# Performance work log

Measured on AMD Instinct MI355X. Metric: run time of the kernel, lower is better.

## Reference

```python
import jax, jax.numpy as jnp
import numpy as np

DIM = 1024
HEADS = 16
SCALE = DIM ** -0.5  # note: source scales by full dim, not head dim


def setup_inputs() -> dict:
    key = jax.random.key(0)
    k1, k2, k3 = jax.random.split(key, 3)
    b, n = 2, 2048
    x = jax.random.normal(k1, (b, n, DIM), dtype=jnp.float32)
    w_qkv = jax.random.normal(k2, (3 * DIM, DIM), dtype=jnp.float32) * (DIM ** -0.5)
    w_out = jax.random.normal(k3, (DIM, DIM), dtype=jnp.float32) * (DIM ** -0.5)
    b_out = jnp.zeros((DIM,), dtype=jnp.float32)
    return {"x": x, "w_qkv": w_qkv, "w_out": w_out, "b_out": b_out}


def reference(x, w_qkv, w_out, b_out):
    b, n, d = x.shape
    h = HEADS
    hd = d // h
    # torch Linear: y = x @ W.T
    qkv = x @ w_qkv.T  # [b, n, 3d]
    q, k, v = jnp.split(qkv, 3, axis=-1)
    # reshape to [b, h, n, hd]
    def to_heads(t):
        return t.reshape(b, n, h, hd).transpose(0, 2, 1, 3)
    q, k, v = to_heads(q), to_heads(k), to_heads(v)
    dots = jnp.einsum('bhqd,bhkd->bhqk', q, k) * SCALE
    attn = jax.nn.softmax(dots, axis=-1)
    out = jnp.einsum('bhqk,bhkd->bhqd', attn, v)
    out = out.transpose(0, 2, 1, 3).reshape(b, n, d)
    return out @ w_out.T + b_out
```

## Files before the change

kernel.cpp:

```cpp
#include <hip/hip_runtime.h>

typedef __attribute__((ext_vector_type(8))) _Float16 half8;
typedef __attribute__((ext_vector_type(4))) _Float16 half4;
typedef __attribute__((ext_vector_type(2))) __fp16 fp16x2;
typedef __attribute__((ext_vector_type(4))) float f32x4;
typedef __attribute__((ext_vector_type(4))) unsigned int u32x4;
typedef __attribute__((ext_vector_type(2))) unsigned int u32x2;

#define NSEQ 2048
#define DIMM 1024
#define NH   16
#define HD   64

typedef const void __attribute__((address_space(1))) gvoid_t;
typedef void __attribute__((address_space(3))) svoid_t;

__device__ __forceinline__ void gload_lds16(const void* g, void* l) {
  __builtin_amdgcn_global_load_lds((gvoid_t*)g, (svoid_t*)l, 16, 0, 0);
}

union H2U { fp16x2 h; unsigned int u; };

__global__ __launch_bounds__(256) void cvt_all(const float* __restrict__ x,
                                               const float* __restrict__ wqkv,
                                               const float* __restrict__ wout,
                                               _Float16* __restrict__ xh,
                                               _Float16* __restrict__ wqkvh,
                                               _Float16* __restrict__ wouth) {
  int i = blockIdx.x * 256 + threadIdx.x;
  const float* src;
  _Float16* dst;
  int off;
  if (i < 524288) { src = x; dst = xh; off = i; }
  else if (i < 917504) { src = wqkv; dst = wqkvh; off = i - 524288; }
  else { src = wout; dst = wouth; off = i - 917504; }
  const float4* p = (const float4*)src + (size_t)off * 2;
  float4 v0 = p[0], v1 = p[1];
  half8 h;
  h[0] = (_Float16)v0.x; h[1] = (_Float16)v0.y; h[2] = (_Float16)v0.z; h[3] = (_Float16)v0.w;
  h[4] = (_Float16)v1.x; h[5] = (_Float16)v1.y; h[6] = (_Float16)v1.z; h[7] = (_Float16)v1.w;
  *((half8*)dst + off) = h;
}

#define QSCALE 0.0450843450f

union SmemQ {
  struct { _Float16 A[3 * 8192]; _Float16 B[3 * 8192]; } m;
  _Float16 t[128 * 264];
};

__global__ __launch_bounds__(512, 1) void gemm_qkv(const _Float16* __restrict__ x,
                                                   const _Float16* __restrict__ wqkv,
                                                   _Float16* __restrict__ qh,
                                                   _Float16* __restrict__ kh,
                                                   _Float16* __restrict__ vt) {
  __shared__ SmemQ sh;
  const int bid = blockIdx.x;
  const int swz = (bid & 7) * 24 + (bid >> 3);
  const int bm = swz & 15, bn = swz >> 4;
  const int am0 = bm * 256, bn0 = bn * 256;
  const int tid = threadIdx.x, w = tid >> 6, lane = tid & 63;
  const int g = lane >> 4, ln = lane & 15;
  const int wmq = (w >> 2) * 128, wnq = (w & 3) * 64;

  const int srl = tid >> 2;
  const int ssl = (tid & 3) ^ ((srl >> 1) & 3);
  const int dsto = tid * 8;

#define QSTG(buf, kt, ht)                                                           \
  {                                                                                 \
    if ((ht) < 2) {                                                                 \
      gload_lds16(x + (size_t)(am0 + (ht) * 128 + srl) * 1024 + (kt) * 32 + ssl * 8,\
                  sh.m.A + (buf) * 8192 + (ht) * 4096 + dsto);                      \
    } else {                                                                        \
      gload_lds16(wqkv + (size_t)(bn0 + ((ht) - 2) * 128 + srl) * 1024 +            \
                      (kt) * 32 + ssl * 8,                                          \
                  sh.m.B + (buf) * 8192 + ((ht) - 2) * 4096 + dsto);                \
    }                                                                               \
  }

  f32x4 acc[8][4];
#pragma unroll
  for (int i = 0; i < 8; ++i)
#pragma unroll
    for (int j = 0; j < 4; ++j) acc[i][j] = (f32x4){0.f, 0.f, 0.f, 0.f};

#pragma unroll
  for (int ht = 0; ht < 4; ++ht) QSTG(0, 0, ht)
#pragma unroll
  for (int ht = 0; ht < 4; ++ht) QSTG(1, 1, ht)

  for (int t = 0; t < 32; ++t) {
    const int buf = t % 3;
    const int sbuf = (t + 2) % 3;
    if (t < 31) {
      asm volatile("s_waitcnt vmcnt(4)" ::: "memory");
    } else {
      asm volatile("s_waitcnt vmcnt(0)" ::: "memory");
    }
    __builtin_amdgcn_s_barrier();
    const _Float16* Ab = sh.m.A + buf * 8192;
    const _Float16* Bb = sh.m.B + buf * 8192;
    half8 bf[4];
#pragma unroll
    for (int ni = 0; ni < 4; ++ni) {
      const int r = wnq + ni * 16 + ln;
      bf[ni] = *(const half8*)(Bb + r * 32 + ((g ^ ((r >> 1) & 3)) << 3));
    }
#pragma unroll
    for (int p = 0; p < 4; ++p) {
      const int r0 = wmq + (2 * p) * 16 + ln;
      const int r1 = wmq + (2 * p + 1) * 16 + ln;
      half8 af0 = *(const half8*)(Ab + r0 * 32 + ((g ^ ((r0 >> 1) & 3)) << 3));
      half8 af1 = *(const half8*)(Ab + r1 * 32 + ((g ^ ((r1 >> 1) & 3)) << 3));
      __builtin_amdgcn_s_setprio(1);
#pragma unroll
      for (int ni = 0; ni < 4; ++ni) {
        acc[2 * p][ni]     = __builtin_amdgcn_mfma_f32_16x16x32_f16(af0, bf[ni], acc[2 * p][ni], 0, 0, 0);
        acc[2 * p + 1][ni] = __builtin_amdgcn_mfma_f32_16x16x32_f16(af1, bf[ni], acc[2 * p + 1][ni], 0, 0, 0);
      }
      __builtin_amdgcn_s_setprio(0);
      if (t < 30) QSTG(sbuf, t + 2, p)
      if (p < 3) __builtin_amdgcn_s_barrier();
    }
  }

  const int sec = bn >> 2;
  const int cbase = (bn & 3) * 256;

  if (sec < 2) {
    _Float16* dst = (sec == 0) ? qh : kh;
    const float scale = (sec == 0) ? QSCALE : 1.0f;
#pragma unroll
    for (int mi = 0; mi < 8; ++mi) {
      const int row = am0 + wmq + mi * 16 + g * 4;
      const int bidx = row >> 11, nidx = row & 2047;
#pragma unroll
      for (int ni = 0; ni < 4; ++ni) {
        const int col = cbase + wnq + ni * 16 + ln;
        const int h = col >> 6, d = col & 63;
        _Float16* p = dst + ((size_t)(bidx * NH + h) * NSEQ + nidx) * HD + d;
#pragma unroll
        for (int r = 0; r < 4; ++r) p[r * HD] = (_Float16)(acc[mi][ni][r] * scale);
      }
    }
  } else {
    const int bidx = bm >> 3;
    const int n0 = (bm * 256) & 2047;
#pragma unroll
    for (int hc = 0; hc < 2; ++hc) {
      __syncthreads();
      if (((w & 3) >> 1) == hc) {
#pragma unroll
        for (int mi = 0; mi < 8; ++mi)
#pragma unroll
          for (int ni = 0; ni < 4; ++ni) {
            const int cl = wnq + ni * 16 + ln - hc * 128;
            const int rowl = wmq + mi * 16 + g * 4;
#pragma unroll
            for (int r = 0; r < 4; ++r)
              sh.t[cl * 264 + rowl + r] = (_Float16)acc[mi][ni][r];
          }
      }
      __syncthreads();
#pragma unroll
      for (int i = 0; i < 8; ++i) {
        const int ci = i * 512 + tid;
        const int cl = ci >> 5, npos = (ci & 31) * 8;
        const int col = cbase + hc * 128 + cl;
        const int h = col >> 6, d = col & 63;
        u32x4 v = *(const u32x4*)(sh.t + cl * 264 + npos);
        *(u32x4*)(vt + ((size_t)(bidx * NH + h) * HD + d) * NSEQ + n0 + npos) = v;
      }
    }
  }
}

__global__ __launch_bounds__(256, 2) void attn_fwd(const _Float16* __restrict__ qg,
                                                   const _Float16* __restrict__ kg,
                                                   const _Float16* __restrict__ vg,
                                                   _Float16* __restrict__ ao) {
  __shared__ _Float16 Ks[3][64 * 64];
  __shared__ _Float16 Vs[3][64 * 64];
  __shared__ float Lred[2][128];

  const int bid = blockIdx.x;
  const int swz = (bid & 7) * 64 + (bid >> 3);
  const int bh = swz >> 4, qt = swz & 15;
  const int tid = threadIdx.x, w = tid >> 6, lane = tid & 63;
  const int g = lane >> 4, ln = lane & 15;
  const int sw8 = ln & 7;
  const int qh2 = w >> 1, kh2 = w & 1;

  const _Float16* qp = qg + (size_t)bh * NSEQ * HD;
  const _Float16* kp = kg + (size_t)bh * NSEQ * HD;
  const _Float16* vp = vg + (size_t)bh * HD * NSEQ;

  const int qr0 = qt * 128;

  half8 qf[4][2];
#pragma unroll
  for (int qb = 0; qb < 4; ++qb)
#pragma unroll
    for (int dk = 0; dk < 2; ++dk)
      qf[qb][dk] = *(const half8*)(qp + (size_t)(qr0 + qh2 * 64 + qb * 16 + ln) * HD + dk * 32 + g * 8);
  asm volatile("" ::: "memory");

  const int rsub = lane >> 3;
  const int csw = ((lane & 7) ^ rsub) << 3;
  const int c0 = 2 * w;
  const int R0 = c0 * 8 + rsub, R1 = R0 + 8;
  const int ks0 = 32 * (R0 >> 5) + 8 * ((R0 >> 2) & 3) + 4 * ((R0 >> 4) & 1) + (R0 & 3);
  const int ks1 = 32 * (R1 >> 5) + 8 * ((R1 >> 2) & 3) + 4 * ((R1 >> 4) & 1) + (R1 & 3);

#define ASTAGE(buf, tt)                                                             \
  {                                                                                 \
    const _Float16* kt_ = kp + (size_t)(tt) * 64 * HD;                              \
    gload_lds16(kt_ + (size_t)ks0 * HD + csw, &Ks[buf][c0 * 512]);                  \
    gload_lds16(kt_ + (size_t)ks1 * HD + csw, &Ks[buf][(c0 + 1) * 512]);            \
    gload_lds16(vp + (size_t)(c0 * 8 + rsub) * NSEQ + (tt) * 64 + csw,              \
                &Vs[buf][c0 * 512]);                                                \
    gload_lds16(vp + (size_t)((c0 + 1) * 8 + rsub) * NSEQ + (tt) * 64 + csw,        \
                &Vs[buf][(c0 + 1) * 512]);                                          \
  }

  ASTAGE(0, 0);
  ASTAGE(1, 1);

  float lsum[4] = {0.f, 0.f, 0.f, 0.f};
  f32x4 oacc[4][4];
#pragma unroll
  for (int sd = 0; sd < 4; ++sd)
#pragma unroll
    for (int qb = 0; qb < 4; ++qb) oacc[sd][qb] = (f32x4){0.f, 0.f, 0.f, 0.f};
  const f32x4 fz = (f32x4){0.f, 0.f, 0.f, 0.f};

#define TILE_BODY(kbuf, vbuf)                                                       \
  {                                                                                 \
    const _Float16* kb_ = (kbuf);                                                   \
    const _Float16* vb_ = (vbuf);                                                   \
    f32x4 sacc[2][4];                                                               \
    __builtin_amdgcn_s_setprio(1);                                                  \
    _Pragma("unroll")                                                               \
    for (int s = 0; s < 2; ++s) {                                                   \
      const _Float16* kr = kb_ + (kh2 * 32 + s * 16 + ln) * 64;                     \
      half8 kf0 = *(const half8*)(kr + ((g ^ sw8) << 3));                           \
      half8 kf1 = *(const half8*)(kr + (((4 + g) ^ sw8) << 3));                     \
      _Pragma("unroll")                                                             \
      for (int qb = 0; qb < 4; ++qb) {                                              \
        sacc[s][qb] = __builtin_amdgcn_mfma_f32_16x16x32_f16(kf0, qf[qb][0], fz, 0, 0, 0);          \
        sacc[s][qb] = __builtin_amdgcn_mfma_f32_16x16x32_f16(kf1, qf[qb][1], sacc[s][qb], 0, 0, 0); \
      }                                                                             \
    }                                                                               \
    __builtin_amdgcn_s_setprio(0);                                                  \
    half8 vf[4];                                                                    \
    _Pragma("unroll")                                                               \
    for (int sd = 0; sd < 4; ++sd)                                                  \
      vf[sd] = *(const half8*)(vb_ + (sd * 16 + ln) * 64 +                          \
                               (((kh2 * 4 + g) ^ sw8) << 3));                       \
    half8 pb[4];                                                                    \
    _Pragma("unroll")                                                               \
    for (int qb = 0; qb < 4; ++qb) {                                                \
      float e0 = __builtin_amdgcn_exp2f(sacc[0][qb][0]);                            \
      float e1 = __builtin_amdgcn_exp2f(sacc[0][qb][1]);                            \
      float e2 = __builtin_amdgcn_exp2f(sacc[0][qb][2]);                            \
      float e3 = __builtin_amdgcn_exp2f(sacc[0][qb][3]);                            \
      float e4 = __builtin_amdgcn_exp2f(sacc[1][qb][0]);                            \
      float e5 = __builtin_amdgcn_exp2f(sacc[1][qb][1]);                            \
      float e6 = __builtin_amdgcn_exp2f(sacc[1][qb][2]);                            \
      float e7 = __builtin_amdgcn_exp2f(sacc[1][qb][3]);                            \
      lsum[qb] += ((e0 + e1) + (e2 + e3)) + ((e4 + e5) + (e6 + e7));                \
      H2U c0_, c1_, c2_, c3_;                                                       \
      c0_.h = __builtin_amdgcn_cvt_pkrtz(e0, e1);                                   \
      c1_.h = __builtin_amdgcn_cvt_pkrtz(e2, e3);                                   \
      c2_.h = __builtin_amdgcn_cvt_pkrtz(e4, e5);                                   \
      c3_.h = __builtin_amdgcn_cvt_pkrtz(e6, e7);                                   \
      union { u32x4 u; half8 h; } pk;                                               \
      pk.u[0] = c0_.u; pk.u[1] = c1_.u; pk.u[2] = c2_.u; pk.u[3] = c3_.u;           \
      pb[qb] = pk.h;                                                                \
    }                                                                               \
    __builtin_amdgcn_s_setprio(1);                                                  \
    _Pragma("unroll")                                                               \
    for (int sd = 0; sd < 4; ++sd)                                                  \
      _Pragma("unroll")                                                             \
      for (int qb = 0; qb < 4; ++qb)                                                \
        oacc[sd][qb] = __builtin_amdgcn_mfma_f32_16x16x32_f16(vf[sd], pb[qb], oacc[sd][qb], 0, 0, 0); \
    __builtin_amdgcn_s_setprio(0);                                                  \
  }

  for (int t = 0; t < 30; ++t) {
    asm volatile("s_waitcnt vmcnt(4)" ::: "memory");
    __builtin_amdgcn_s_barrier();
    ASTAGE((t + 2) % 3, t + 2);
    TILE_BODY(&Ks[t % 3][0], &Vs[t % 3][0])
  }
  {
    asm volatile("s_waitcnt vmcnt(4)" ::: "memory");
    __builtin_amdgcn_s_barrier();
    TILE_BODY(&Ks[0][0], &Vs[0][0])
  }
  {
    asm volatile("s_waitcnt vmcnt(0)" ::: "memory");
    __builtin_amdgcn_s_barrier();
    TILE_BODY(&Ks[1][0], &Vs[1][0])
  }

#pragma unroll
  for (int qb = 0; qb < 4; ++qb) {
    lsum[qb] += __shfl_xor(lsum[qb], 16, 64);
    lsum[qb] += __shfl_xor(lsum[qb], 32, 64);
  }
  __syncthreads();
  float* Osh = (float*)&Ks[0][0];
  if (g == 0) {
#pragma unroll
    for (int qb = 0; qb < 4; ++qb)
      Lred[kh2][qh2 * 64 + qb * 16 + ln] = lsum[qb];
  }
  if (kh2) {
#pragma unroll
    for (int sd = 0; sd < 4; ++sd)
#pragma unroll
      for (int qb = 0; qb < 4; ++qb)
        *(f32x4*)&Osh[(qh2 * 64 + qb * 16 + ln) * 66 + sd * 16 + g * 4] = oacc[sd][qb];
  }
  __syncthreads();
  if (!kh2) {
    const int bidx = bh >> 4, h = bh & 15;
#pragma unroll
    for (int qb = 0; qb < 4; ++qb) {
      const int q = qh2 * 64 + qb * 16 + ln;
      const float inv = 1.f / (Lred[0][q] + Lred[1][q]);
      const int n = qr0 + q;
#pragma unroll
      for (int sd = 0; sd < 4; ++sd) {
        f32x4 part = *(const f32x4*)&Osh[q * 66 + sd * 16 + g * 4];
        half4 o4;
#pragma unroll
        for (int r = 0; r < 4; ++r) o4[r] = (_Float16)((oacc[sd][qb][r] + part[r]) * inv);
        *(half4*)(ao + (size_t)(bidx * NSEQ + n) * DIMM + h * HD + sd * 16 + g * 4) = o4;
      }
    }
  }
}

__global__ __launch_bounds__(256) void gemm_out(const _Float16* __restrict__ ao,
                                                const _Float16* __restrict__ wout,
                                                const float* __restrict__ bias,
                                                float* __restrict__ out) {
  __shared__ _Float16 As[3 * 128 * 32];
  __shared__ _Float16 Bs[3 * 64 * 32];
  f32x4 acc[4][2];
#pragma unroll
  for (int i = 0; i < 4; ++i)
#pragma unroll
    for (int j = 0; j < 2; ++j) acc[i][j] = (f32x4){0.f, 0.f, 0.f, 0.f};
  const int bm = blockIdx.x, bn = blockIdx.y;
  const int am0 = bm * 128, bn0 = bn * 64;

  const int tid = threadIdx.x;
  const int w = tid >> 6, lane = tid & 63;
  const int lr = lane >> 2;
  const int cc = (lane & 3) ^ ((lr >> 1) & 3);
  const int wm = (w >> 1) * 64, wn = (w & 1) * 32;
  const int g = lane >> 4, ln = lane & 15;

#define GSTAGE_O(buf, kk)                                                           \
  {                                                                                 \
    _Pragma("unroll")                                                               \
    for (int i = 0; i < 3; ++i) {                                                   \
      int c = w * 3 + i;                                                            \
      if (c < 8) {                                                                  \
        gload_lds16(ao + (size_t)(am0 + c * 16 + lr) * 1024 + (kk) + cc * 8,        \
                    As + (buf) * 4096 + c * 512);                                   \
      } else {                                                                      \
        int cb = c - 8;                                                             \
        gload_lds16(wout + (size_t)(bn0 + cb * 16 + lr) * 1024 + (kk) + cc * 8,     \
                    Bs + (buf) * 2048 + cb * 512);                                  \
      }                                                                             \
    }                                                                               \
  }

  GSTAGE_O(0, 0)
  GSTAGE_O(1, 32)
  for (int t = 0; t < 32; ++t) {
    if (t < 31) {
      asm volatile("s_waitcnt vmcnt(3)" ::: "memory");
    } else {
      asm volatile("s_waitcnt vmcnt(0)" ::: "memory");
    }
    __builtin_amdgcn_s_barrier();
    if (t < 30) GSTAGE_O((t + 2) % 3, (t + 2) * 32);
    const _Float16* as_ = As + (t % 3) * 4096;
    const _Float16* bs_ = Bs + (t % 3) * 2048;
    half8 af[4], bf[2];
#pragma unroll
    for (int mi = 0; mi < 4; ++mi) {
      const int r = wm + mi * 16 + ln;
      af[mi] = *(const half8*)(as_ + r * 32 + ((g ^ ((r >> 1) & 3)) << 3));
    }
#pragma unroll
    for (int ni = 0; ni < 2; ++ni) {
      const int r = wn + ni * 16 + ln;
      bf[ni] = *(const half8*)(bs_ + r * 32 + ((g ^ ((r >> 1) & 3)) << 3));
    }
#pragma unroll
    for (int mi = 0; mi < 4; ++mi)
#pragma unroll
      for (int ni = 0; ni < 2; ++ni)
        acc[mi][ni] = __builtin_amdgcn_mfma_f32_16x16x32_f16(af[mi], bf[ni], acc[mi][ni], 0, 0, 0);
  }

#pragma unroll
  for (int mi = 0; mi < 4; ++mi) {
    const int row = bm * 128 + wm + mi * 16 + g * 4;
#pragma unroll
    for (int ni = 0; ni < 2; ++ni) {
      const int col = bn * 64 + wn + ni * 16 + ln;
      const float b = bias[col];
#pragma unroll
      for (int r = 0; r < 4; ++r) out[(size_t)(row + r) * DIMM + col] = acc[mi][ni][r] + b;
    }
  }
}

extern "C" void kernel_launch(void* const* d_in, const int* in_sizes, int n_in,
                              void* d_out, int out_size, void* d_ws, size_t ws_size,
                              hipStream_t stream) {
  const float* x    = (const float*)d_in[0];
  const float* wqkv = (const float*)d_in[1];
  const float* wout = (const float*)d_in[2];
  const float* bout = (const float*)d_in[3];
  float* out = (float*)d_out;

  _Float16* ws = (_Float16*)d_ws;
  _Float16* x_h    = ws;
  _Float16* wqkv_h = ws + (4u << 20);
  _Float16* wout_h = ws + (7u << 20);
  _Float16* q_h    = ws + (8u << 20);
  _Float16* k_h    = ws + (12u << 20);
  _Float16* vt_h   = ws + (16u << 20);
  _Float16* ao_h   = ws + (20u << 20);

  cvt_all<<<dim3(4096), 256, 0, stream>>>(x, wqkv, wout, x_h, wqkv_h, wout_h);
  gemm_qkv<<<dim3(192), 512, 0, stream>>>(x_h, wqkv_h, q_h, k_h, vt_h);
  attn_fwd<<<dim3(512), 256, 0, stream>>>(q_h, k_h, vt_h, ao_h);
  gemm_out<<<dim3(32, 16), 256, 0, stream>>>(ao_h, wout_h, bout, out);
}
```

Measured before the change: 100.4 us.

## Switch attention K/V staging to double-buffered 128-key tiles

Replaces the triple-buffered 64-key K/V ring with a double buffer of 128-key tiles, halving the number of barrier and wait points per key sweep. V is now loaded with a 128-wide row stride and a new XOR swizzle. Each 128-key tile is processed as two 64-key sub-tiles. The cost is a full vmcnt(0) wait before each tile, with only one tile in flight instead of two, which may expose global-load latency.

Result: no change. 100.5 us (+0.1%).

```diff
diff --git a/kernel.cpp b/kernel.cpp
--- a/kernel.cpp
+++ b/kernel.cpp
@@ -180,8 +180,7 @@
                                                    const _Float16* __restrict__ kg,
                                                    const _Float16* __restrict__ vg,
                                                    _Float16* __restrict__ ao) {
-  __shared__ _Float16 Ks[3][64 * 64];
-  __shared__ _Float16 Vs[3][64 * 64];
+  __shared__ _Float16 KV[2][16384];
   __shared__ float Lred[2][128];
 
   const int bid = blockIdx.x;
@@ -208,24 +207,33 @@
 
   const int rsub = lane >> 3;
   const int csw = ((lane & 7) ^ rsub) << 3;
-  const int c0 = 2 * w;
-  const int R0 = c0 * 8 + rsub, R1 = R0 + 8;
-  const int ks0 = 32 * (R0 >> 5) + 8 * ((R0 >> 2) & 3) + 4 * ((R0 >> 4) & 1) + (R0 & 3);
-  const int ks1 = 32 * (R1 >> 5) + 8 * ((R1 >> 2) & 3) + 4 * ((R1 >> 4) & 1) + (R1 & 3);
+  const int c0k = 4 * w;
+  const int Rk0 = c0k * 8 + rsub, Rk1 = Rk0 + 8, Rk2 = Rk0 + 16, Rk3 = Rk0 + 24;
+#define KSRC(R) (32 * ((R) >> 5) + 8 * (((R) >> 2) & 3) + 4 * (((R) >> 4) & 1) + ((R) & 3))
+  const int ks0 = KSRC(Rk0), ks1 = KSRC(Rk1), ks2 = KSRC(Rk2), ks3 = KSRC(Rk3);
+
+  const int rv = lane >> 4;
+  const int sl = lane & 15;
+  const int rd0 = c0k * 4 + rv;
+  const int rd1 = rd0 + 4;
+  const int vsA = (sl ^ (rd0 & 7)) * 8;
+  const int vsB = (sl ^ (rd1 & 7)) * 8;
 
 #define ASTAGE(buf, tt)                                                             \
   {                                                                                 \
-    const _Float16* kt_ = kp + (size_t)(tt) * 64 * HD;                              \
-    gload_lds16(kt_ + (size_t)ks0 * HD + csw, &Ks[buf][c0 * 512]);                  \
-    gload_lds16(kt_ + (size_t)ks1 * HD + csw, &Ks[buf][(c0 + 1) * 512]);            \
-    gload_lds16(vp + (size_t)(c0 * 8 + rsub) * NSEQ + (tt) * 64 + csw,              \
-                &Vs[buf][c0 * 512]);                                                \
-    gload_lds16(vp + (size_t)((c0 + 1) * 8 + rsub) * NSEQ + (tt) * 64 + csw,        \
-                &Vs[buf][(c0 + 1) * 512]);                                          \
+    const _Float16* kt_ = kp + (size_t)(tt) * 128 * HD;                             \
+    gload_lds16(kt_ + (size_t)ks0 * HD + csw, &KV[buf][(c0k + 0) * 512]);           \
+    gload_lds16(kt_ + (size_t)ks1 * HD + csw, &KV[buf][(c0k + 1) * 512]);           \
+    gload_lds16(kt_ + (size_t)ks2 * HD + csw, &KV[buf][(c0k + 2) * 512]);           \
+    gload_lds16(kt_ + (size_t)ks3 * HD + csw, &KV[buf][(c0k + 3) * 512]);           \
+    const _Float16* vt_ = vp + (size_t)(tt) * 128;                                  \
+    gload_lds16(vt_ + (size_t)(rd0)     * NSEQ + vsA, &KV[buf][8192 + (c0k + 0) * 512]); \
+    gload_lds16(vt_ + (size_t)(rd0 + 4) * NSEQ + vsB, &KV[buf][8192 + (c0k + 1) * 512]); \
+    gload_lds16(vt_ + (size_t)(rd0 + 8) * NSEQ + vsA, &KV[buf][8192 + (c0k + 2) * 512]); \
+    gload_lds16(vt_ + (size_t)(rd0 +12) * NSEQ + vsB, &KV[buf][8192 + (c0k + 3) * 512]); \
   }
 
   ASTAGE(0, 0);
-  ASTAGE(1, 1);
 
   float lsum[4] = {0.f, 0.f, 0.f, 0.f};
   f32x4 oacc[4][4];
@@ -235,7 +243,7 @@
     for (int qb = 0; qb < 4; ++qb) oacc[sd][qb] = (f32x4){0.f, 0.f, 0.f, 0.f};
   const f32x4 fz = (f32x4){0.f, 0.f, 0.f, 0.f};
 
-#define TILE_BODY(kbuf, vbuf)                                                       \
+#define TILE_SUB(kbuf, vbuf, SUB)                                                   \
   {                                                                                 \
     const _Float16* kb_ = (kbuf);                                                   \
     const _Float16* vb_ = (vbuf);                                                   \
@@ -243,7 +251,7 @@
     __builtin_amdgcn_s_setprio(1);                                                  \
     _Pragma("unroll")                                                               \
     for (int s = 0; s < 2; ++s) {                                                   \
-      const _Float16* kr = kb_ + (kh2 * 32 + s * 16 + ln) * 64;                     \
+      const _Float16* kr = kb_ + ((SUB) * 64 + kh2 * 32 + s * 16 + ln) * 64;        \
       half8 kf0 = *(const half8*)(kr + ((g ^ sw8) << 3));                           \
       half8 kf1 = *(const half8*)(kr + (((4 + g) ^ sw8) << 3));                     \
       _Pragma("unroll")                                                             \
@@ -253,11 +261,11 @@
       }                                                                             \
     }                                                                               \
     __builtin_amdgcn_s_setprio(0);                                                  \
-    half8 vf[4];                                                                    \
+    half8 vf[4];                 \
     _Pragma("unroll")                                                               \
     for (int sd = 0; sd < 4; ++sd)                                                  \
-      vf[sd] = *(const half8*)(vb_ + (sd * 16 + ln) * 64 +                          \
-                               (((kh2 * 4 + g) ^ sw8) << 3));                       \
+      vf[sd] = *(const half8*)(vb_ + (sd * 16 + ln) * 128 +                         \
+                               ((((SUB) * 8 + kh2 * 4 + g) ^ sw8) << 3));           \
     half8 pb[4];                                                                    \
     _Pragma("unroll")                                                               \
     for (int qb = 0; qb < 4; ++qb) {                                                \
@@ -288,21 +296,18 @@
     __builtin_amdgcn_s_setprio(0);                                                  \
   }
 
-  for (int t = 0; t < 30; ++t) {
-    asm volatile("s_waitcnt vmcnt(4)" ::: "memory");
+  for (int t = 0; t < 15; ++t) {
+    asm volatile("s_waitcnt vmcnt(0)" ::: "memory");
     __builtin_amdgcn_s_barrier();
-    ASTAGE((t + 2) % 3, t + 2);
-    TILE_BODY(&Ks[t % 3][0], &Vs[t % 3][0])
-  }
-  {
-    asm volatile("s_waitcnt vmcnt(4)" ::: "memory");
-    __builtin_amdgcn_s_barrier();
-    TILE_BODY(&Ks[0][0], &Vs[0][0])
+    ASTAGE((t + 1) & 1, t + 1);
+    TILE_SUB(&KV[t & 1][0], &KV[t & 1][8192], 0)
+    TILE_SUB(&KV[t & 1][0], &KV[t & 1][8192], 1)
   }
   {
     asm volatile("s_waitcnt vmcnt(0)" ::: "memory");
     __builtin_amdgcn_s_barrier();
-    TILE_BODY(&Ks[1][0], &Vs[1][0])
+    TILE_SUB(&KV[1][0], &KV[1][8192], 0)
+    TILE_SUB(&KV[1][0], &KV[1][8192], 1)
   }
 
 #pragma unroll
@@ -311,7 +316,7 @@
     lsum[qb] += __shfl_xor(lsum[qb], 32, 64);
   }
   __syncthreads();
-  float* Osh = (float*)&Ks[0][0];
+  float* Osh = (float*)&KV[0][0];
   if (g == 0) {
 #pragma unroll
     for (int qb = 0; qb < 4; ++qb)
```
